# Performance work log

Measured on AMD Instinct MI355X. Metric: run time of the kernel, lower is better.

## Reference

```python
import jax, jax.numpy as jnp
import numpy as np
import math

HIDDEN = 1024
HEADS = 16
HEAD_DIM = HIDDEN // HEADS
B, S = 4, 4096


def setup_inputs() -> dict:
    key = jax.random.key(0)
    ks = jax.random.split(key, 9)
    std = 1.0 / math.sqrt(HIDDEN)
    mk = lambda k: (jax.random.normal(k, (HIDDEN, HIDDEN), jnp.float32) * std)
    return {
        "x": jax.random.normal(ks[0], (B, S, HIDDEN), jnp.float32),
        "Wq": mk(ks[1]), "bq": jnp.zeros((HIDDEN,), jnp.float32),
        "Wk": mk(ks[2]), "bk": jnp.zeros((HIDDEN,), jnp.float32),
        "Wv": mk(ks[3]), "bv": jnp.zeros((HIDDEN,), jnp.float32),
        "Wo": mk(ks[4]), "bo": jnp.zeros((HIDDEN,), jnp.float32),
    }


def reference(x, Wq, bq, Wk, bk, Wv, bv, Wo, bo):
    b, s, _ = x.shape
    scale = 1.0 / math.sqrt(HEAD_DIM)
    # projections: [b, s, hidden] -> [b, heads, s, head_dim]
    def proj(W, bias):
        y = jnp.einsum('bsh,hd->bsd', x, W.T) + bias  # torch Linear: x @ W.T + b
        return y.reshape(b, s, HEADS, HEAD_DIM).transpose(0, 2, 1, 3)
    q = proj(Wq, bq)
    k = proj(Wk, bk)
    v = proj(Wv, bv)
    # FFT along sequence axis (axis=2)
    q_f = jnp.fft.rfft(q, axis=2)
    k_f = jnp.fft.rfft(k, axis=2)
    v_f = jnp.fft.rfft(v, axis=2)
    out_f = q_f * jnp.conj(k_f) * v_f
    out = jnp.fft.irfft(out_f, n=s, axis=2) * scale
    out = out.transpose(0, 2, 1, 3).reshape(b, s, HIDDEN)
    out = jnp.einsum('bsh,hd->bsd', out, Wo.T) + bo
    # dropout is identity in eval mode
    return out
```

## Files before the change

### kernel.cpp

```cpp
#include <hip/hip_runtime.h>
#include <hip/hip_bf16.h>
#include <math.h>

#define HIDDEN   1024
#define HEADS    16
#define HEAD_DIM 64
#define BATCH    4
#define SEQ      4096
#define M_TOTAL  (BATCH * SEQ)
#define FFT_N    4096
#define WSZ      ((size_t)HIDDEN * HIDDEN)
#define PI2      6.28318530717958647692f

typedef _Float16 f16x8 __attribute__((ext_vector_type(8)));
typedef float    f32x4 __attribute__((ext_vector_type(4)));

#if defined(__has_builtin)
#if __has_builtin(__builtin_amdgcn_global_load_lds)
#define HAVE_GLL 1
#else
#define HAVE_GLL 0
#endif
#else
#define HAVE_GLL 0
#endif

#if HAVE_GLL
__device__ __forceinline__ void gload16(const void* g, void* l) {
    __builtin_amdgcn_global_load_lds(
        (const __attribute__((address_space(1))) unsigned int*)g,
        (__attribute__((address_space(3))) unsigned int*)l,
        16, 0, 0);
}
#endif

__device__ __forceinline__ void cvt8_f16(float4 v0, float4 v1,
                                         ushort* __restrict__ d) {
    const float vv[8] = {v0.x, v0.y, v0.z, v0.w, v1.x, v1.y, v1.z, v1.w};
    f16x8 hv;
    #pragma unroll
    for (int e = 0; e < 8; ++e) hv[e] = (_Float16)vv[e];
    *(f16x8*)d = hv;
}

__global__ __launch_bounds__(256) void cvt16_kernel(
    const float* __restrict__ src, ushort* __restrict__ h)
{
    const size_t i = ((size_t)blockIdx.x * 256 + threadIdx.x) * 8;
    float4 v0 = *(const float4*)(src + i);
    float4 v1 = *(const float4*)(src + i + 4);
    cvt8_f16(v0, v1, h + i);
}

__global__ __launch_bounds__(256) void cvtW_kernel(
    const float* __restrict__ Wq, const float* __restrict__ Wk,
    const float* __restrict__ Wv, const float* __restrict__ Wo,
    ushort* __restrict__ wh, ushort* __restrict__ woh)
{
    const int p = blockIdx.y;
    const size_t i = ((size_t)blockIdx.x * 256 + threadIdx.x) * 8;
    const float* __restrict__ src = (p == 0) ? Wq : (p == 1 ? Wk : (p == 2 ? Wv : Wo));
    ushort* __restrict__ dst = (p < 3) ? (wh + (size_t)p * WSZ) : woh;
    float4 v0 = *(const float4*)(src + i);
    float4 v1 = *(const float4*)(src + i + 4);
    cvt8_f16(v0, v1, dst + i);
}

__global__ __launch_bounds__(1024, 1) void gemm_qkv_mfma8(
    const ushort* __restrict__ xh, const ushort* __restrict__ wh,
    const float* __restrict__ bq, const float* __restrict__ bk,
    const float* __restrict__ bv,
    ushort* __restrict__ qkvt)
{
    __shared__ ushort Ah[3][8192];
    __shared__ ushort Bh[3][8192];

    const int tid  = threadIdx.x;
    const int lane = tid & 63;
    const int wid  = tid >> 6;
    const int wr   = wid >> 2;
    const int wc   = wid & 3;
    const int m0   = blockIdx.x * 256;
    const int ng0  = blockIdx.y * 256;
    const int p    = ng0 >> 10;
    const int n0p  = ng0 & 1023;

    const float* __restrict__ bias = (p == 0) ? bq : (p == 1 ? bk : bv);
    ushort* __restrict__ ct = qkvt + (size_t)p * HIDDEN * M_TOTAL;

    const int row = tid >> 2;
    const int chS = (tid & 3) ^ ((row >> 1) & 3);

    const int fr = lane & 15;
    const int fc = lane >> 4;
    const int cc = (fc ^ ((fr >> 1) & 3)) * 8;

    f32x4 acc[4][4];
    #pragma unroll
    for (int rf = 0; rf < 4; ++rf)
        #pragma unroll
        for (int cf = 0; cf < 4; ++cf)
            acc[rf][cf] = (f32x4){0.f, 0.f, 0.f, 0.f};

#if HAVE_GLL
    #define QKV_STAGE(K0, SLOT) {                                                  \
        const size_t gw = (size_t)(ng0 + row) * HIDDEN + (K0) + (size_t)chS * 8;   \
        const size_t gx = (size_t)(m0 + row) * HIDDEN + (K0) + (size_t)chS * 8;    \
        gload16(wh + gw, &Ah[SLOT][(size_t)tid * 8]);                              \
        gload16(xh + gx, &Bh[SLOT][(size_t)tid * 8]);                              \
    }
#else
    #define QKV_STAGE(K0, SLOT) {                                                  \
        const size_t gw = (size_t)(ng0 + row) * HIDDEN + (K0) + (size_t)chS * 8;   \
        const size_t gx = (size_t)(m0 + row) * HIDDEN + (K0) + (size_t)chS * 8;    \
        *(f16x8*)&Ah[SLOT][(size_t)tid * 8] = *(const f16x8*)(wh + gw);            \
        *(f16x8*)&Bh[SLOT][(size_t)tid * 8] = *(const f16x8*)(xh + gx);            \
    }
#endif

    QKV_STAGE(0, 0);
    QKV_STAGE(32, 1);

    for (int ks = 0; ks < 32; ++ks) {
        const int slot = ks % 3;
#if HAVE_GLL
        if (ks == 31) { asm volatile("s_waitcnt vmcnt(0)" ::: "memory"); }
        else          { asm volatile("s_waitcnt vmcnt(2)" ::: "memory"); }
        __builtin_amdgcn_s_barrier();
        asm volatile("" ::: "memory");
#else
        __syncthreads();
#endif
        {
            const ushort* pAh = Ah[slot];
            const ushort* pBh = Bh[slot];
            f16x8 a_h[4], b_h[4];
            #pragma unroll
            for (int rf = 0; rf < 4; ++rf) {
                const int R = wr * 64 + rf * 16 + fr;
                a_h[rf] = *(const f16x8*)(pAh + R * 32 + cc);
            }
            #pragma unroll
            for (int cf = 0; cf < 4; ++cf) {
                const int R = wc * 64 + cf * 16 + fr;
                b_h[cf] = *(const f16x8*)(pBh + R * 32 + cc);
            }
            #pragma unroll
            for (int rf = 0; rf < 4; ++rf)
                #pragma unroll
                for (int cf = 0; cf < 4; ++cf)
                    acc[rf][cf] = __builtin_amdgcn_mfma_f32_16x16x32_f16(a_h[rf], b_h[cf], acc[rf][cf], 0, 0, 0);
        }
        if (ks + 2 < 32) { QKV_STAGE((ks + 2) * 32, (ks + 2) % 3); }
#if !HAVE_GLL
        __syncthreads();
#endif
    }
    #undef QKV_STAGE

    const int rq = lane >> 4;
    #pragma unroll
    for (int rf = 0; rf < 4; ++rf) {
        #pragma unroll
        for (int r = 0; r < 4; ++r) {
            const int nl = wr * 64 + rf * 16 + rq * 4 + r;
            const float bv = bias[n0p + nl];
            ushort* dst = ct + (size_t)(n0p + nl) * M_TOTAL + m0 + wc * 64;
            #pragma unroll
            for (int cf = 0; cf < 4; ++cf) {
                union { _Float16 f; ushort u; } cvt;
                cvt.f = (_Float16)(acc[rf][cf][r] + bv);
                dst[cf * 16 + fr] = cvt.u;
            }
        }
    }
}

__device__ __forceinline__ float2 cmul(float2 a, float2 b) {
    return {a.x*b.x - a.y*b.y, a.x*b.y + a.y*b.x};
}

__device__ __forceinline__ int phys(int p) { return p ^ ((p >> 4) & 15); }

__device__ __forceinline__ unsigned pk16(float2 v) {
    union { _Float16 f[2]; unsigned u; } c;
    c.f[0] = (_Float16)v.x; c.f[1] = (_Float16)v.y;
    return c.u;
}
__device__ __forceinline__ float2 upk16(unsigned u) {
    union { unsigned uu; _Float16 f[2]; } c; c.uu = u;
    return (float2){(float)c.f[0], (float)c.f[1]};
}

template<int DIR>
__device__ __forceinline__ void dft16(const float2* x, float2* X) {
    float2 t[16];
    #pragma unroll
    for (int n0 = 0; n0 < 4; ++n0) {
        float2 a = x[n0], b = x[n0+4], c = x[n0+8], d = x[n0+12];
        float2 s0 = {a.x+c.x, a.y+c.y}, s1 = {a.x-c.x, a.y-c.y};
        float2 s2 = {b.x+d.x, b.y+d.y}, s3 = {b.x-d.x, b.y-d.y};
        t[n0*4+0] = {s0.x+s2.x, s0.y+s2.y};
        t[n0*4+2] = {s0.x-s2.x, s0.y-s2.y};
        if (DIR < 0) {
            t[n0*4+1] = {s1.x+s3.y, s1.y-s3.x};
            t[n0*4+3] = {s1.x-s3.y, s1.y+s3.x};
        } else {
            t[n0*4+1] = {s1.x-s3.y, s1.y+s3.x};
            t[n0*4+3] = {s1.x+s3.y, s1.y-s3.x};
        }
    }
    const float C1 = 0.92387953251128674f;
    const float S1_ = 0.38268343236508978f;
    const float R2 = 0.70710678118654752f;
    #define TW(idx, cc_, ss_) t[idx] = cmul(t[idx], (float2){cc_, DIR*(ss_)})
    TW(1*4+1, C1, S1_);   TW(1*4+2, R2, R2);    TW(1*4+3, S1_, C1);
    TW(2*4+1, R2, R2);    TW(2*4+2, 0.f, 1.f);  TW(2*4+3, -R2, R2);
    TW(3*4+1, S1_, C1);   TW(3*4+2, -R2, R2);   TW(3*4+3, -C1, -S1_);
    #undef TW
    #pragma unroll
    for (int k0 = 0; k0 < 4; ++k0) {
        float2 a = t[0+k0], b = t[4+k0], c = t[8+k0], d = t[12+k0];
        float2 s0 = {a.x+c.x, a.y+c.y}, s1 = {a.x-c.x, a.y-c.y};
        float2 s2 = {b.x+d.x, b.y+d.y}, s3 = {b.x-d.x, b.y-d.y};
        X[k0+0]  = {s0.x+s2.x, s0.y+s2.y};
        X[k0+8]  = {s0.x-s2.x, s0.y-s2.y};
        if (DIR < 0) {
            X[k0+4]  = {s1.x+s3.y, s1.y-s3.x};
            X[k0+12] = {s1.x-s3.y, s1.y+s3.x};
        } else {
            X[k0+4]  = {s1.x-s3.y, s1.y+s3.x};
            X[k0+12] = {s1.x+s3.y, s1.y-s3.x};
        }
    }
}

__device__ __forceinline__ void twiddle_apply(float2* y, float ang) {
    float s, c;
    __sincosf(ang, &s, &c);
    const float2 base = {c, s};
    float2 w = base;
    #pragma unroll
    for (int u = 1; u < 16; ++u) {
        y[u] = cmul(y[u], w);
        w = cmul(w, base);
    }
}

__global__ __launch_bounds__(256) void fft_attn_kernel2(
    const ushort* __restrict__ qt, const ushort* __restrict__ kt,
    const ushort* __restrict__ vt, ushort* __restrict__ ot16)
{
    __shared__ unsigned zA[2][FFT_N];
    __shared__ float2 bufB[FFT_N];

    const int tid = threadIdx.x;
    const int bid = blockIdx.x;
    const int n   = bid >> 1;
    const int bp  = bid & 1;

    const size_t off0 = (size_t)n * M_TOTAL + (size_t)(2 * bp) * SEQ;
    const size_t off1 = off0 + SEQ;
    const _Float16* q0 = (const _Float16*)qt + off0;
    const _Float16* k0 = (const _Float16*)kt + off0;
    const _Float16* q1 = (const _Float16*)qt + off1;
    const _Float16* k1 = (const _Float16*)kt + off1;
    const _Float16* v0 = (const _Float16*)vt + off0;
    const _Float16* v1 = (const _Float16*)vt + off1;
    _Float16* o0 = (_Float16*)ot16 + off0;
    _Float16* o1 = (_Float16*)ot16 + off1;

    {
        const float ang = -PI2 * (float)tid / 4096.f;
        {
            float2 x[16], y[16];
            #pragma unroll
            for (int r = 0; r < 16; ++r)
                x[r] = { (float)q0[tid + 256*r], (float)k0[tid + 256*r] };
            dft16<-1>(x, y);
            twiddle_apply(y, ang);
            #pragma unroll
            for (int u = 0; u < 16; ++u) zA[0][phys(tid + 256*u)] = pk16(y[u]);
        }
        {
            float2 x[16], y[16];
            #pragma unroll
            for (int r = 0; r < 16; ++r)
                x[r] = { (float)q1[tid + 256*r], (float)k1[tid + 256*r] };
            dft16<-1>(x, y);
            twiddle_apply(y, ang);
            #pragma unroll
            for (int u = 0; u < 16; ++u) zA[1][phys(tid + 256*u)] = pk16(y[u]);
        }
        {
            float2 x[16], y[16];
            #pragma unroll
            for (int r = 0; r < 16; ++r)
                x[r] = { (float)v0[tid + 256*r], (float)v1[tid + 256*r] };
            dft16<-1>(x, y);
            twiddle_apply(y, ang);
            #pragma unroll
            for (int u = 0; u < 16; ++u) bufB[phys(tid + 256*u)] = y[u];
        }
    }
    __syncthreads();
    {
        const int blk = tid >> 4, a = tid & 15;
        const int base = 256*blk + a;
        const float ang = -PI2 * (float)a / 256.f;
        #pragma unroll
        for (int d = 0; d < 2; ++d) {
            float2 x[16], y[16];
            #pragma unroll
            for (int c = 0; c < 16; ++c) x[c] = upk16(zA[d][phys(base + 16*c)]);
            dft16<-1>(x, y);
            twiddle_apply(y, ang);
            #pragma unroll
            for (int c = 0; c < 16; ++c) zA[d][phys(base + 16*c)] = pk16(y[c]);
        }
        {
            float2 x[16], y[16];
            #pragma unroll
            for (int c = 0; c < 16; ++c) x[c] = bufB[phys(base + 16*c)];
            dft16<-1>(x, y);
            twiddle_apply(y, ang);
            #pragma unroll
            for (int c = 0; c < 16; ++c) bufB[phys(base + 16*c)] = y[c];
        }
    }
    __syncthreads();
    {
        const int base = 256*(tid >> 4) + 16*(tid & 15);
        #pragma unroll
        for (int d = 0; d < 2; ++d) {
            float2 x[16], y[16];
            #pragma unroll
            for (int e = 0; e < 16; ++e) x[e] = upk16(zA[d][phys(base + e)]);
            dft16<-1>(x, y);
            #pragma unroll
            for (int e = 0; e < 16; ++e) zA[d][phys(base + e)] = pk16(y[e]);
        }
        {
            float2 x[16], y[16];
            #pragma unroll
            for (int e = 0; e < 16; ++e) x[e] = bufB[phys(base + e)];
            dft16<-1>(x, y);
            #pragma unroll
            for (int e = 0; e < 16; ++e) bufB[phys(base + e)] = y[e];
        }
    }
    __syncthreads();
    float2 H[16];
    #pragma unroll
    for (int it = 0; it < 16; ++it) {
        const int p  = tid + it * 256;
        const int j  = ((p & 15) << 8) | (p & 0xF0) | (p >> 8);
        const int jn = (FFT_N - j) & (FFT_N - 1);
        const int pn = ((jn & 15) << 8) | (jn & 0xF0) | (jn >> 8);
        const float2 Vj = bufB[phys(p)];
        const float2 Vn = bufB[phys(pn)];
        const float2 V1 = { 0.5f*(Vj.x + Vn.x),  0.5f*(Vj.y - Vn.y) };
        const float2 V2 = { 0.5f*(Vj.y + Vn.y), -0.5f*(Vj.x - Vn.x) };
        float2 F1, F2;
        {
            const float2 Zj = upk16(zA[0][phys(p)]);
            const float2 Zn = upk16(zA[0][phys(pn)]);
            const float2 Q = { 0.5f*(Zj.x + Zn.x),  0.5f*(Zj.y - Zn.y) };
            const float2 K = { 0.5f*(Zj.y + Zn.y), -0.5f*(Zj.x - Zn.x) };
            const float2 G = { Q.x*K.x + Q.y*K.y, Q.y*K.x - Q.x*K.y };
            F1 = { G.x*V1.x - G.y*V1.y, G.x*V1.y + G.y*V1.x };
        }
        {
            const float2 Zj = upk16(zA[1][phys(p)]);
            const float2 Zn = upk16(zA[1][phys(pn)]);
            const float2 Q = { 0.5f*(Zj.x + Zn.x),  0.5f*(Zj.y - Zn.y) };
            const float2 K = { 0.5f*(Zj.y + Zn.y), -0.5f*(Zj.x - Zn.x) };
            const float2 G = { Q.x*K.x + Q.y*K.y, Q.y*K.x - Q.x*K.y };
            F2 = { G.x*V2.x - G.y*V2.y, G.x*V2.y + G.y*V2.x };
        }
        H[it] = { F1.x - F2.y, F1.y + F2.x };
    }
    __syncthreads();
    #pragma unroll
    for (int it = 0; it < 16; ++it)
        bufB[phys(tid + it * 256)] = H[it];
    __syncthreads();
    {
        const int base = 256*(tid >> 4) + 16*(tid & 15);
        float2 x[16], y[16];
        #pragma unroll
        for (int d = 0; d < 16; ++d) x[d] = bufB[phys(base + d)];
        dft16<1>(x, y);
        #pragma unroll
        for (int p0 = 0; p0 < 16; ++p0) bufB[phys(base + p0)] = y[p0];
    }
    __syncthreads();
    {
        const int blk = tid >> 4, p0 = tid & 15;
        const int base = 256*blk + p0;
        float2 x[16], y[16];
        #pragma unroll
        for (int c = 0; c < 16; ++c) x[c] = bufB[phys(base + 16*c)];
        twiddle_apply(x, PI2 * (float)p0 / 256.f);
        dft16<1>(x, y);
        #pragma unroll
        for (int p1 = 0; p1 < 16; ++p1) bufB[phys(base + 16*p1)] = y[p1];
    }
    __syncthreads();
    {
        const int qq = tid;
        float2 x[16], y[16];
        #pragma unroll
        for (int t = 0; t < 16; ++t) x[t] = bufB[phys(qq + 256*t)];
        twiddle_apply(x, PI2 * (float)qq / 4096.f);
        dft16<1>(x, y);
        const float scale = 0.125f / 4096.f;
        #pragma unroll
        for (int p2 = 0; p2 < 16; ++p2) {
            o0[qq + 256*p2] = (_Float16)(y[p2].x * scale);
            o1[qq + 256*p2] = (_Float16)(y[p2].y * scale);
        }
    }
}

__global__ __launch_bounds__(256) void transpose_cvt_kernel(
    const ushort* __restrict__ ot, ushort* __restrict__ oth)
{
    __shared__ float tile[64][65];
    const int tid = threadIdx.x;
    const int m0  = blockIdx.x * 64;
    const int n0  = blockIdx.y * 64;
    const int r   = tid >> 4;
    const int c   = tid & 15;

    #pragma unroll
    for (int rr = 0; rr < 4; ++rr) {
        const int nl = r + rr * 16;
        ushort4 v = *(const ushort4*)(ot + (size_t)(n0 + nl) * M_TOTAL + m0 + c * 4);
        union { ushort u; _Float16 f; } cv;
        cv.u = v.x; tile[nl][c * 4 + 0] = (float)cv.f;
        cv.u = v.y; tile[nl][c * 4 + 1] = (float)cv.f;
        cv.u = v.z; tile[nl][c * 4 + 2] = (float)cv.f;
        cv.u = v.w; tile[nl][c * 4 + 3] = (float)cv.f;
    }
    __syncthreads();
    #pragma unroll
    for (int rr = 0; rr < 4; ++rr) {
        const int ml = r + rr * 16;
        ushort4 hh;
        union { _Float16 f; ushort u; } cv;
        cv.f = (_Float16)tile[c * 4 + 0][ml]; hh.x = cv.u;
        cv.f = (_Float16)tile[c * 4 + 1][ml]; hh.y = cv.u;
        cv.f = (_Float16)tile[c * 4 + 2][ml]; hh.z = cv.u;
        cv.f = (_Float16)tile[c * 4 + 3][ml]; hh.w = cv.u;
        *(ushort4*)(oth + (size_t)(m0 + ml) * HIDDEN + n0 + c * 4) = hh;
    }
}

__global__ __launch_bounds__(1024, 1) void gemm_out_mfma8(
    const ushort* __restrict__ oth, const ushort* __restrict__ woh,
    const float* __restrict__ bo, float* __restrict__ out)
{
    __shared__ ushort Ah[3][8192];
    __shared__ ushort Bh[3][8192];

    const int tid  = threadIdx.x;
    const int lane = tid & 63;
    const int wid  = tid >> 6;
    const int wr   = wid >> 2;
    const int wc   = wid & 3;
    const int m0   = blockIdx.x * 256;
    const int n0   = blockIdx.y * 256;

    const int row = tid >> 2;
    const int chS = (tid & 3) ^ ((row >> 1) & 3);

    const int fr = lane & 15;
    const int fc = lane >> 4;
    const int cc = (fc ^ ((fr >> 1) & 3)) * 8;

    f32x4 acc[4][4];
    #pragma unroll
    for (int rf = 0; rf < 4; ++rf)
        #pragma unroll
        for (int cf = 0; cf < 4; ++cf)
            acc[rf][cf] = (f32x4){0.f, 0.f, 0.f, 0.f};

#if HAVE_GLL
    #define OUT_STAGE(K0, SLOT) {                                                  \
        const size_t ga = (size_t)(m0 + row) * HIDDEN + (K0) + (size_t)chS * 8;    \
        const size_t gb = (size_t)(n0 + row) * HIDDEN + (K0) + (size_t)chS * 8;    \
        gload16(oth + ga, &Ah[SLOT][(size_t)tid * 8]);                             \
        gload16(woh + gb, &Bh[SLOT][(size_t)tid * 8]);                             \
    }
#else
    #define OUT_STAGE(K0, SLOT) {                                                  \
        const size_t ga = (size_t)(m0 + row) * HIDDEN + (K0) + (size_t)chS * 8;    \
        const size_t gb = (size_t)(n0 + row) * HIDDEN + (K0) + (size_t)chS * 8;    \
        *(f16x8*)&Ah[SLOT][(size_t)tid * 8] = *(const f16x8*)(oth + ga);           \
        *(f16x8*)&Bh[SLOT][(size_t)tid * 8] = *(const f16x8*)(woh + gb);           \
    }
#endif

    OUT_STAGE(0, 0);
    OUT_STAGE(32, 1);

    for (int ks = 0; ks < 32; ++ks) {
        const int slot = ks % 3;
#if HAVE_GLL
        if (ks == 31) { asm volatile("s_waitcnt vmcnt(0)" ::: "memory"); }
        else          { asm volatile("s_waitcnt vmcnt(2)" ::: "memory"); }
        __builtin_amdgcn_s_barrier();
        asm volatile("" ::: "memory");
#else
        __syncthreads();
#endif
        {
            const ushort* pAh = Ah[slot];
            const ushort* pBh = Bh[slot];
            f16x8 a_h[4], b_h[4];
            #pragma unroll
            for (int rf = 0; rf < 4; ++rf) {
                const int R = wr * 64 + rf * 16 + fr;
                a_h[rf] = *(const f16x8*)(pAh + R * 32 + cc);
            }
            #pragma unroll
            for (int cf = 0; cf < 4; ++cf) {
                const int R = wc * 64 + cf * 16 + fr;
                b_h[cf] = *(const f16x8*)(pBh + R * 32 + cc);
            }
            #pragma unroll
            for (int rf = 0; rf < 4; ++rf)
                #pragma unroll
                for (int cf = 0; cf < 4; ++cf)
                    acc[rf][cf] = __builtin_amdgcn_mfma_f32_16x16x32_f16(a_h[rf], b_h[cf], acc[rf][cf], 0, 0, 0);
        }
        if (ks + 2 < 32) { OUT_STAGE((ks + 2) * 32, (ks + 2) % 3); }
#if !HAVE_GLL
        __syncthreads();
#endif
    }
    #undef OUT_STAGE

    const int rq = lane >> 4;
    float bo_v[4];
    #pragma unroll
    for (int cf = 0; cf < 4; ++cf) bo_v[cf] = bo[n0 + wc * 64 + cf * 16 + fr];
    #pragma unroll
    for (int rf = 0; rf < 4; ++rf) {
        #pragma unroll
        for (int r = 0; r < 4; ++r) {
            const int ml = wr * 64 + rf * 16 + rq * 4 + r;
            float* dst = out + (size_t)(m0 + ml) * HIDDEN + n0 + wc * 64;
            #pragma unroll
            for (int cf = 0; cf < 4; ++cf)
                dst[cf * 16 + fr] = acc[rf][cf][r] + bo_v[cf];
        }
    }
}

extern "C" void kernel_launch(void* const* d_in, const int* in_sizes, int n_in,
                              void* d_out, int out_size, void* d_ws, size_t ws_size,
                              hipStream_t stream)
{
    const float* x  = (const float*)d_in[0];
    const float* Wq = (const float*)d_in[1];
    const float* bq = (const float*)d_in[2];
    const float* Wk = (const float*)d_in[3];
    const float* bk = (const float*)d_in[4];
    const float* Wv = (const float*)d_in[5];
    const float* bv = (const float*)d_in[6];
    const float* Wo = (const float*)d_in[7];
    const float* bo = (const float*)d_in[8];
    float* out = (float*)d_out;

    const size_t plane = (size_t)HIDDEN * M_TOTAL;
    ushort* qkvt = (ushort*)d_ws;
    ushort* qt16 = qkvt;
    ushort* kt16 = qkvt + plane;
    ushort* vt16 = qkvt + 2 * plane;
    ushort* ot16 = qkvt + 3 * plane;
    ushort* woh  = ot16 + plane;

    ushort* oth = qkvt;

    ushort* xh  = (ushort*)d_out;
    ushort* wh  = xh + plane;

    cvt16_kernel<<<(unsigned)(plane / 2048), 256, 0, stream>>>(x, xh);
    cvtW_kernel<<<dim3((unsigned)(WSZ / 2048), 4), 256, 0, stream>>>(
        Wq, Wk, Wv, Wo, wh, woh);

    gemm_qkv_mfma8<<<dim3(M_TOTAL / 256, 12), 1024, 0, stream>>>(
        xh, wh, bq, bk, bv, qkvt);

    fft_attn_kernel2<<<dim3(HIDDEN * BATCH / 2), 256, 0, stream>>>(
        qt16, kt16, vt16, ot16);

    transpose_cvt_kernel<<<dim3(M_TOTAL / 64, HIDDEN / 64), 256, 0, stream>>>(
        ot16, oth);

    gemm_out_mfma8<<<dim3(M_TOTAL / 256, HIDDEN / 256), 1024, 0, stream>>>(
        oth, woh, bo, out);
}
```

Before: 249.2 us.

## Split FFT attention work across three 256-thread groups per block

The FFT attention kernel now launches 768 threads per block. Each 256-thread group handles one of the three forward FFTs (q0/k0, q1/k1, v) in parallel instead of one group doing all three sequentially, and the spectral product is spread across the groups. The aim is more parallelism per block and shorter serial per-thread work. The inverse FFT stages run only on group 0, which leaves two thirds of the threads idle there, and the larger block may lower the number of resident blocks per CU.

```diff
diff --git a/kernel.cpp b/kernel.cpp
--- a/kernel.cpp
+++ b/kernel.cpp
@@ -247,7 +247,7 @@
     }
 }
 
-__global__ __launch_bounds__(256) void fft_attn_kernel2(
+__global__ __launch_bounds__(768) void fft_attn_kernel3(
     const ushort* __restrict__ qt, const ushort* __restrict__ kt,
     const ushort* __restrict__ vt, ushort* __restrict__ ot16)
 {
@@ -255,6 +255,8 @@
     __shared__ float2 bufB[FFT_N];
 
     const int tid = threadIdx.x;
+    const int g   = tid >> 8;
+    const int lt  = tid & 255;
     const int bid = blockIdx.x;
     const int n   = bid >> 1;
     const int bp  = bid & 1;
@@ -271,122 +273,117 @@
     _Float16* o1 = (_Float16*)ot16 + off1;
 
     {
-        const float ang = -PI2 * (float)tid / 4096.f;
-        {
-            float2 x[16], y[16];
+        const float ang = -PI2 * (float)lt / 4096.f;
+        float2 x[16], y[16];
+        if (g == 0) {
             #pragma unroll
             for (int r = 0; r < 16; ++r)
-                x[r] = { (float)q0[tid + 256*r], (float)k0[tid + 256*r] };
-            dft16<-1>(x, y);
-            twiddle_apply(y, ang);
-            #pragma unroll
-            for (int u = 0; u < 16; ++u) zA[0][phys(tid + 256*u)] = pk16(y[u]);
-        }
-        {
-            float2 x[16], y[16];
+                x[r] = { (float)q0[lt + 256*r], (float)k0[lt + 256*r] };
+        } else if (g == 1) {
             #pragma unroll
             for (int r = 0; r < 16; ++r)
-                x[r] = { (float)q1[tid + 256*r], (float)k1[tid + 256*r] };
-            dft16<-1>(x, y);
-            twiddle_apply(y, ang);
-            #pragma unroll
-            for (int u = 0; u < 16; ++u) zA[1][phys(tid + 256*u)] = pk16(y[u]);
-        }
-        {
-            float2 x[16], y[16];
+                x[r] = { (float)q1[lt + 256*r], (float)k1[lt + 256*r] };
+        } else {
             #pragma unroll
             for (int r = 0; r < 16; ++r)
-                x[r] = { (float)v0[tid + 256*r], (float)v1[tid + 256*r] };
-            dft16<-1>(x, y);
-            twiddle_apply(y, ang);
-            #pragma unroll
-            for (int u = 0; u < 16; ++u) bufB[phys(tid + 256*u)] = y[u];
+                x[r] = { (float)v0[lt + 256*r], (float)v1[lt + 256*r] };
+        }
+        dft16<-1>(x, y);
+        twiddle_apply(y, ang);
+        if (g < 2) {
+            #pragma unroll
+            for (int u = 0; u < 16; ++u) zA[g][phys(lt + 256*u)] = pk16(y[u]);
+        } else {
+            #pragma unroll
+            for (int u = 0; u < 16; ++u) bufB[phys(lt + 256*u)] = y[u];
         }
     }
     __syncthreads();
     {
-        const int blk = tid >> 4, a = tid & 15;
+        const int blk = lt >> 4, a = lt & 15;
         const int base = 256*blk + a;
         const float ang = -PI2 * (float)a / 256.f;
-        #pragma unroll
-        for (int d = 0; d < 2; ++d) {
-            float2 x[16], y[16];
-            #pragma unroll
-            for (int c = 0; c < 16; ++c) x[c] = upk16(zA[d][phys(base + 16*c)]);
-            dft16<-1>(x, y);
-            twiddle_apply(y, ang);
-            #pragma unroll
-            for (int c = 0; c < 16; ++c) zA[d][phys(base + 16*c)] = pk16(y[c]);
-        }
-        {
-            float2 x[16], y[16];
+        float2 x[16], y[16];
+        if (g < 2) {
+            #pragma unroll
+            for (int c = 0; c < 16; ++c) x[c] = upk16(zA[g][phys(base + 16*c)]);
+        } else {
             #pragma unroll
             for (int c = 0; c < 16; ++c) x[c] = bufB[phys(base + 16*c)];
-            dft16<-1>(x, y);
-            twiddle_apply(y, ang);
+        }
+        dft16<-1>(x, y);
+        twiddle_apply(y, ang);
+        if (g < 2) {
+            #pragma unroll
+            for (int c = 0; c < 16; ++c) zA[g][phys(base + 16*c)] = pk16(y[c]);
+        } else {
             #pragma unroll
             for (int c = 0; c < 16; ++c) bufB[phys(base + 16*c)] = y[c];
         }
     }
     __syncthreads();
     {
-        const int base = 256*(tid >> 4) + 16*(tid & 15);
-        #pragma unroll
-        for (int d = 0; d < 2; ++d) {
-            float2 x[16], y[16];
-            #pragma unroll
-            for (int e = 0; e < 16; ++e) x[e] = upk16(zA[d][phys(base + e)]);
-            dft16<-1>(x, y);
-            #pragma unroll
-            for (int e = 0; e < 16; ++e) zA[d][phys(base + e)] = pk16(y[e]);
-        }
-        {
-            float2 x[16], y[16];
+        const int base = 256*(lt >> 4) + 16*(lt & 15);
+        float2 x[16], y[16];
+        if (g < 2) {
+            #pragma unroll
+            for (int e = 0; e < 16; ++e) x[e] = upk16(zA[g][phys(base + e)]);
+        } else {
             #pragma unroll
             for (int e = 0; e < 16; ++e) x[e] = bufB[phys(base + e)];
-            dft16<-1>(x, y);
+        }
+        dft16<-1>(x, y);
+        if (g < 2) {
+            #pragma unroll
+            for (int e = 0; e < 16; ++e) zA[g][phys(base + e)] = pk16(y[e]);
+        } else {
             #pragma unroll
             for (int e = 0; e < 16; ++e) bufB[phys(base + e)] = y[e];
         }
     }
     __syncthreads();
-    float2 H[16];
-    #pragma unroll
-    for (int it = 0; it < 16; ++it) {
-        const int p  = tid + it * 256;
-        const int j  = ((p & 15) << 8) | (p & 0xF0) | (p >> 8);
-        const int jn = (FFT_N - j) & (FFT_N - 1);
-        const int pn = ((jn & 15) << 8) | (jn & 0xF0) | (jn >> 8);
-        const float2 Vj = bufB[phys(p)];
-        const float2 Vn = bufB[phys(pn)];
-        const float2 V1 = { 0.5f*(Vj.x + Vn.x),  0.5f*(Vj.y - Vn.y) };
-        const float2 V2 = { 0.5f*(Vj.y + Vn.y), -0.5f*(Vj.x - Vn.x) };
-        float2 F1, F2;
-        {
-            const float2 Zj = upk16(zA[0][phys(p)]);
-            const float2 Zn = upk16(zA[0][phys(pn)]);
-            const float2 Q = { 0.5f*(Zj.x + Zn.x),  0.5f*(Zj.y - Zn.y) };
-            const float2 K = { 0.5f*(Zj.y + Zn.y), -0.5f*(Zj.x - Zn.x) };
-            const float2 G = { Q.x*K.x + Q.y*K.y, Q.y*K.x - Q.x*K.y };
-            F1 = { G.x*V1.x - G.y*V1.y, G.x*V1.y + G.y*V1.x };
-        }
-        {
-            const float2 Zj = upk16(zA[1][phys(p)]);
-            const float2 Zn = upk16(zA[1][phys(pn)]);
-            const float2 Q = { 0.5f*(Zj.x + Zn.x),  0.5f*(Zj.y - Zn.y) };
-            const float2 K = { 0.5f*(Zj.y + Zn.y), -0.5f*(Zj.x - Zn.x) };
-            const float2 G = { Q.x*K.x + Q.y*K.y, Q.y*K.x - Q.x*K.y };
-            F2 = { G.x*V2.x - G.y*V2.y, G.x*V2.y + G.y*V2.x };
-        }
-        H[it] = { F1.x - F2.y, F1.y + F2.x };
-    }
-    __syncthreads();
-    #pragma unroll
-    for (int it = 0; it < 16; ++it)
-        bufB[phys(tid + it * 256)] = H[it];
-    __syncthreads();
-    {
-        const int base = 256*(tid >> 4) + 16*(tid & 15);
+    float2 H[6];
+    #pragma unroll
+    for (int it = 0; it < 6; ++it) {
+        const int s = g + 3 * it;
+        if (s < 16) {
+            const int p  = lt + s * 256;
+            const int j  = ((p & 15) << 8) | (p & 0xF0) | (p >> 8);
+            const int jn = (FFT_N - j) & (FFT_N - 1);
+            const int pn = ((jn & 15) << 8) | (jn & 0xF0) | (jn >> 8);
+            const float2 Vj = bufB[phys(p)];
+            const float2 Vn = bufB[phys(pn)];
+            const float2 V1 = { 0.5f*(Vj.x + Vn.x),  0.5f*(Vj.y - Vn.y) };
+            const float2 V2 = { 0.5f*(Vj.y + Vn.y), -0.5f*(Vj.x - Vn.x) };
+            float2 F1, F2;
+            {
+                const float2 Zj = upk16(zA[0][phys(p)]);
+                const float2 Zn = upk16(zA[0][phys(pn)]);
+                const float2 Q = { 0.5f*(Zj.x + Zn.x),  0.5f*(Zj.y - Zn.y) };
+                const float2 K = { 0.5f*(Zj.y + Zn.y), -0.5f*(Zj.x - Zn.x) };
+                const float2 G = { Q.x*K.x + Q.y*K.y, Q.y*K.x - Q.x*K.y };
+                F1 = { G.x*V1.x - G.y*V1.y, G.x*V1.y + G.y*V1.x };
+            }
+            {
+                const float2 Zj = upk16(zA[1][phys(p)]);
+                const float2 Zn = upk16(zA[1][phys(pn)]);
+                const float2 Q = { 0.5f*(Zj.x + Zn.x),  0.5f*(Zj.y - Zn.y) };
+                const float2 K = { 0.5f*(Zj.y + Zn.y), -0.5f*(Zj.x - Zn.x) };
+                const float2 G = { Q.x*K.x + Q.y*K.y, Q.y*K.x - Q.x*K.y };
+                F2 = { G.x*V2.x - G.y*V2.y, G.x*V2.y + G.y*V2.x };
+            }
+            H[it] = { F1.x - F2.y, F1.y + F2.x };
+        }
+    }
+    __syncthreads();
+    #pragma unroll
+    for (int it = 0; it < 6; ++it) {
+        const int s = g + 3 * it;
+        if (s < 16) bufB[phys(lt + s * 256)] = H[it];
+    }
+    __syncthreads();
+    if (g == 0) {
+        const int base = 256*(lt >> 4) + 16*(lt & 15);
         float2 x[16], y[16];
         #pragma unroll
         for (int d = 0; d < 16; ++d) x[d] = bufB[phys(base + d)];
@@ -395,8 +392,8 @@
         for (int p0 = 0; p0 < 16; ++p0) bufB[phys(base + p0)] = y[p0];
     }
     __syncthreads();
-    {
-        const int blk = tid >> 4, p0 = tid & 15;
+    if (g == 0) {
+        const int blk = lt >> 4, p0 = lt & 15;
         const int base = 256*blk + p0;
         float2 x[16], y[16];
         #pragma unroll
@@ -407,8 +404,8 @@
         for (int p1 = 0; p1 < 16; ++p1) bufB[phys(base + 16*p1)] = y[p1];
     }
     __syncthreads();
-    {
-        const int qq = tid;
+    if (g == 0) {
+        const int qq = lt;
         float2 x[16], y[16];
         #pragma unroll
         for (int t = 0; t < 16; ++t) x[t] = bufB[phys(qq + 256*t)];
@@ -594,7 +591,7 @@
     gemm_qkv_mfma8<<<dim3(M_TOTAL / 256, 12), 1024, 0, stream>>>(
         xh, wh, bq, bk, bv, qkvt);
 
-    fft_attn_kernel2<<<dim3(HIDDEN * BATCH / 2), 256, 0, stream>>>(
+    fft_attn_kernel3<<<dim3(HIDDEN * BATCH / 2), 768, 0, stream>>>(
         qt16, kt16, vt16, ot16);
 
     transpose_cvt_kernel<<<dim3(M_TOTAL / 64, HIDDEN / 64), 256, 0, stream>>>(
```

Measured after the change: 266.0 us. 1.07x slower.
